# Kernel optimization log

Hardware: AMD Instinct MI355X
Metric: run time of the kernel (lower is better)

## Reference

```python
import jax, jax.numpy as jnp
import numpy as np

N, T, D, H = 100000, 16, 8, 40
HP1 = H + 1
ALPHA_DP = 1.0
KAPPA0 = 1000.0   # priorGaussianVarKappa
NU0 = 100.0       # priorWishartNu
PSI0_SCALE = 500.0  # priorWishartPsi = 500*I


def setup_inputs() -> dict:
    key = jax.random.key(0)
    ks = jax.random.split(key, 6)
    return {
        "BetaGamma1": jnp.ones((1, T), jnp.float32),
        "Phi": jax.random.uniform(ks[0], (N, T), jnp.float32),
        "inputData": jax.random.normal(ks[1], (N, D), jnp.float32),
        "outputData": jax.random.normal(ks[2], (N, 1), jnp.float32),
        "weightELM": jax.random.uniform(ks[3], (D, H), jnp.float32) * 2.0 - 1.0,
        "biasELM": jax.random.normal(ks[4], (H, 1), jnp.float32),
        "epsilonA": jnp.ones((1, T), jnp.float32),
        "epsilonB": jnp.ones((1, T), jnp.float32),
        "zetaA": 1e-4 * jnp.ones((1, T), jnp.float32),
        "zetaB": jnp.ones((1, T), jnp.float32),
    }


def reference(BetaGamma1, Phi, inputData, outputData, weightELM, biasELM,
              epsilonA, epsilonB, zetaA, zetaB):
    f32 = jnp.float32
    mu0 = jnp.zeros((D, 1), f32)                      # priorGaussianMeanMu
    Psi0 = PSI0_SCALE * jnp.eye(D, dtype=f32)         # priorWishartPsi

    sumPhi = jnp.sum(Phi, axis=0, keepdims=True)      # [1,T]

    # stick-breaking Beta params. Torch builds a flipped [T,N,T] tril mask;
    # mathematically BetaGamma2[t] = alpha + sum_{j>t} sum_n Phi[n,j]
    BetaGamma1_new = jnp.ones_like(BetaGamma1) + sumPhi
    col = sumPhi[0]                                   # [T]
    rev_incl = jnp.cumsum(col[::-1])[::-1]            # sum_{j>=t}
    BetaGamma2 = (ALPHA_DP + (rev_incl - col))[None, :]

    # Gaussian-Wishart natural-parameter updates.
    # Torch loops over clusters doing [N,D,D] bmm outer products; this is
    # S[:,:,t] = sum_n Phi[n,t] x_n x_n^T
    S = jnp.einsum('nt,ni,nj->ijt', Phi, inputData, inputData)  # [D,D,T]
    t11 = -0.5 * (Psi0 + KAPPA0 * mu0 @ mu0.T)[:, :, None] - 0.5 * S
    t12 = KAPPA0 * mu0 + inputData.T @ Phi            # [D,T]
    t21 = -0.5 * sumPhi - 0.5 * (NU0 + D + 2)         # [1,T]
    kappa = KAPPA0 + sumPhi                           # [1,T]
    mu = t12 / kappa                                  # [D,T]
    nu = -2.0 * t21 - 2.0 - float(D)                  # [1,T]
    psi = -2.0 * t11 - kappa[0][None, None, :] * jnp.einsum('it,jt->ijt', mu, mu)

    # ELM feature map + augmented design matrix X = [sigmoid(x W + b), 1]
    hmap = jax.nn.sigmoid(inputData @ weightELM + biasELM.T)   # [N,H]
    X = jnp.concatenate([hmap, jnp.ones((inputData.shape[0], 1), f32)], axis=1)  # [N,HP1]

    epsExp = (epsilonA / epsilonB)[0]                 # [T]
    zetaExp = (zetaA / zetaB)[0]                      # [T]

    # A[t] = X^T diag(Phi[:,t]) X   (torch: per-cluster bmm with diag_embed)
    A = jnp.einsum('nt,ni,nj->tij', Phi, X, X)        # [T,HP1,HP1]
    WS = jnp.linalg.inv(epsExp[:, None, None] * A
                        + zetaExp[:, None, None] * jnp.eye(HP1, dtype=f32))
    # b[t] = X^T diag(Phi[:,t]) y
    b = jnp.einsum('ni,nt->ti', X * outputData, Phi)  # [T,HP1]
    WMv = zetaExp[:, None] * jnp.einsum('tij,tj->ti', WS, b)   # [T,HP1]
    WM = WMv[:, :, None]                              # [T,HP1,1]

    # prior Zeta/Epsilon alias the variational initial values in __init__
    zetaA_new = zetaA + (H + 1) * 0.5
    zetaB_new = zetaB + 0.5 * (jnp.sum(WMv * WMv, axis=1)
                               + jnp.trace(WS, axis1=-2, axis2=-1))[None, :]
    epsA_new = epsilonA + 0.5 * sumPhi

    pred = jnp.einsum('ni,ti->tn', X, WMv)            # [T,N]
    err = outputData.T - pred                          # [T,N]
    t1 = jnp.einsum('tn,nt->t', err * err, Phi)[None, :]
    t2 = jnp.einsum('tij,tji->t', A, WS)[None, :]
    epsB_new = epsilonB + 0.5 * (t1 + t2)

    return (BetaGamma1_new, BetaGamma2, mu, kappa, nu, psi,
            WM, WS, zetaA_new, zetaB_new, epsA_new, epsB_new)
```

## Files before the change

kernel.cpp:

```cpp
#include <hip/hip_runtime.h>

#define Nn 100000
#define Tt 16
#define Dd 8
#define Hh 40
#define HP1 41

#define CSZ 53248
#define XEH_OFF  0
#define XEL_OFF  (XEH_OFF + 32 * Nn)
#define PHIT_OFF (XEL_OFF + 32 * Nn)
#define PART_OFF (PHIT_OFF + 16 * Nn)
#define P_OFF    (PART_OFF + 8 * CSZ)

#define OFF_BG1   0
#define OFF_BG2   16
#define OFF_MU    32
#define OFF_KAPPA 160
#define OFF_NU    176
#define OFF_PSI   192
#define OFF_WM    1216
#define OFF_WS    1872
#define OFF_ZA    28768
#define OFF_ZB    28784
#define OFF_EA    28800
#define OFF_EB    28816

typedef _Float16 f16x8 __attribute__((ext_vector_type(8)));
typedef float f32x4 __attribute__((ext_vector_type(4)));
typedef unsigned int u32x4 __attribute__((ext_vector_type(4)));

#define AIDX(i, t, j) ((((i) * 16 + (t)) * 64) + (j))

__global__ __launch_bounds__(256)
void elm_expand(const float* __restrict__ Phi, const float* __restrict__ Xd,
                const float* __restrict__ Yd, const float* __restrict__ W,
                const float* __restrict__ bb,
                unsigned short* __restrict__ XeHi, unsigned short* __restrict__ XeLo,
                float* __restrict__ PhiT)
{
  __shared__ float sW[Dd * Hh];
  __shared__ float sb[Hh];
  __shared__ float xs[64][9];
  __shared__ float ys[64];
  __shared__ float hrow[64][41];
  __shared__ float pt[16][68];
  int tid = threadIdx.x;
  int n0 = blockIdx.x * 64;

  for (int i = tid; i < Dd * Hh; i += 256) sW[i] = W[i];
  if (tid < Hh) sb[tid] = bb[tid];
  if (tid < 128) {
    int nl = tid >> 1, h4 = (tid & 1) * 4;
    int gn = n0 + nl;
    float4 v = (gn < Nn) ? *(const float4*)(Xd + (size_t)gn * 8 + h4)
                         : make_float4(0.f, 0.f, 0.f, 0.f);
    xs[nl][h4 + 0] = v.x; xs[nl][h4 + 1] = v.y;
    xs[nl][h4 + 2] = v.z; xs[nl][h4 + 3] = v.w;
  }
  if (tid < 64) { int gn = n0 + tid; ys[tid] = (gn < Nn) ? Yd[gn] : 0.f; }
  {
    int nl = tid >> 2, q = tid & 3;
    int gn = n0 + nl;
    float4 v = (gn < Nn) ? *(const float4*)(Phi + (size_t)gn * 16 + q * 4)
                         : make_float4(0.f, 0.f, 0.f, 0.f);
    pt[q * 4 + 0][nl] = v.x; pt[q * 4 + 1][nl] = v.y;
    pt[q * 4 + 2][nl] = v.z; pt[q * 4 + 3][nl] = v.w;
  }
  __syncthreads();
  {
    int nl = tid >> 2, hq = (tid & 3) * 10;
    for (int hh = 0; hh < 10; ++hh) {
      int h = hq + hh;
      float z = sb[h];
#pragma unroll
      for (int d = 0; d < 8; ++d) z = fmaf(xs[nl][d], sW[d * Hh + h], z);
      hrow[nl][h] = 1.f / (1.f + __expf(-z));
    }
  }
  __syncthreads();
  {
    int t = tid & 15, nq = tid >> 4;
    int gn = n0 + nq * 4;
    if (gn < Nn) {
      float4 v = make_float4(pt[t][nq * 4 + 0], pt[t][nq * 4 + 1],
                             pt[t][nq * 4 + 2], pt[t][nq * 4 + 3]);
      *(float4*)(PhiT + (size_t)t * Nn + gn) = v;
    }
  }
  {
    int cidx = tid >> 2, seg = tid & 3;
    int nl0 = seg * 16;
    float vv[16];
#pragma unroll
    for (int j = 0; j < 16; ++j) {
      int n = nl0 + j;
      float v;
      if (cidx < Hh) v = hrow[n][cidx];
      else if (cidx == 40) v = 1.f;
      else if (cidx < 49) v = xs[n][cidx - 41];
      else if (cidx == 49) v = ys[n];
      else v = 0.f;
      vv[j] = v;
    }
    unsigned short hs[16], ls[16];
#pragma unroll
    for (int j = 0; j < 16; ++j) {
      _Float16 h = (_Float16)vv[j];
      float r = vv[j] - (float)h;
      _Float16 lo = (_Float16)r;
      hs[j] = __builtin_bit_cast(unsigned short, h);
      ls[j] = __builtin_bit_cast(unsigned short, lo);
    }
#pragma unroll
    for (int q2 = 0; q2 < 2; ++q2) {
      int gn = n0 + nl0 + q2 * 8;
      if (gn < Nn) {
        uint4 uh, ul;
        uh.x = hs[q2*8+0] | ((unsigned)hs[q2*8+1] << 16);
        uh.y = hs[q2*8+2] | ((unsigned)hs[q2*8+3] << 16);
        uh.z = hs[q2*8+4] | ((unsigned)hs[q2*8+5] << 16);
        uh.w = hs[q2*8+6] | ((unsigned)hs[q2*8+7] << 16);
        ul.x = ls[q2*8+0] | ((unsigned)ls[q2*8+1] << 16);
        ul.y = ls[q2*8+2] | ((unsigned)ls[q2*8+3] << 16);
        ul.z = ls[q2*8+4] | ((unsigned)ls[q2*8+5] << 16);
        ul.w = ls[q2*8+6] | ((unsigned)ls[q2*8+7] << 16);
        *(uint4*)(XeHi + (size_t)cidx * Nn + gn) = uh;
        *(uint4*)(XeLo + (size_t)cidx * Nn + gn) = ul;
      }
    }
  }
}

__device__ __forceinline__ void gload16(const void* g, void* l) {
  __builtin_amdgcn_global_load_lds(
      (const __attribute__((address_space(1))) unsigned int*)g,
      (__attribute__((address_space(3))) unsigned int*)l, 16, 0, 0);
}

__global__ __launch_bounds__(512, 2)
void gram_mfma(const float* __restrict__ PhiT,
               const unsigned short* __restrict__ XeHi,
               const unsigned short* __restrict__ XeLo,
               float* __restrict__ P, int CH)
{
  __shared__ __align__(16) char smem[2][10240];

  int tid = threadIdx.x;
  int c = blockIdx.x;
  int l = tid & 63, w = tid >> 6;
  int l15 = l & 15, lg = l >> 4;
  int n0 = c * CH;
  int rem = Nn - n0; if (rem > CH) rem = CH;
  int nsteps = rem >> 5;

  int MT  = (w < 4) ? 7 : 6;
  int i0w = (w < 4) ? 7 * w : 28 + 6 * (w - 4);

  const char* g0; const char* g1 = nullptr;
  int ld0 = tid * 16, ld1 = (512 + tid) * 16;
  {
    int r = (tid & 255) >> 2, s = tid & 3;
    const unsigned short* bp = (tid < 256) ? XeHi : XeLo;
    g0 = (const char*)(bp + (size_t)r * Nn + n0 + 8 * (s ^ (r & 3)));
    if (tid < 128) {
      int t = tid >> 3, s2 = tid & 7;
      g1 = (const char*)(PhiT + (size_t)t * Nn + n0 + 4 * (s2 ^ (t & 7)));
    }
  }

#define STAGE(buf) do {                              \
    char* db = &smem[buf][0];                        \
    gload16(g0, db + ld0); g0 += 64;                 \
    if (tid < 128) { gload16(g1, db + ld1); g1 += 128; } \
  } while (0)

  int off_b[4];
#pragma unroll
  for (int nt = 0; nt < 4; ++nt) {
    int j = l15 + 16 * nt;
    off_b[nt] = j * 64 + 16 * (lg ^ (j & 3));
  }
  int off_p0 = 8192 + l15 * 128 + 16 * ((2 * lg) ^ (l15 & 7));
  int off_p1 = 8192 + l15 * 128 + 16 * ((2 * lg + 1) ^ (l15 & 7));
  int off_a[7];
#pragma unroll
  for (int mi = 0; mi < 7; ++mi) {
    int i = i0w + mi;
    off_a[mi] = i * 64 + 16 * (lg ^ (i & 3));
  }

  f32x4 acc[7][4];
#pragma unroll
  for (int mi = 0; mi < 7; ++mi)
#pragma unroll
    for (int nt = 0; nt < 4; ++nt) acc[mi][nt] = (f32x4){0.f, 0.f, 0.f, 0.f};

  STAGE(0);
  __syncthreads();

  for (int s = 0; s < nsteps; ++s) {
    int cur = s & 1;
    if (s + 1 < nsteps) STAGE(cur ^ 1);

    const char* base = &smem[cur][0];
    f32x4 p0 = *(const f32x4*)(base + off_p0);
    f32x4 p1 = *(const f32x4*)(base + off_p1);
    float ph[8] = {p0[0], p0[1], p0[2], p0[3], p1[0], p1[1], p1[2], p1[3]};

    f16x8 bh[4], bl[4];
#pragma unroll
    for (int nt = 0; nt < 4; ++nt) {
      bh[nt] = *(const f16x8*)(base + off_b[nt]);
      bl[nt] = *(const f16x8*)(base + 4096 + off_b[nt]);
    }
#pragma unroll
    for (int mi = 0; mi < 7; ++mi) {
      if (mi >= MT) break;
      f16x8 xh = *(const f16x8*)(base + off_a[mi]);
      f16x8 xl = *(const f16x8*)(base + 4096 + off_a[mi]);
      float v0 = ph[0] * ((float)xh[0] + (float)xl[0]);
      float v1 = ph[1] * ((float)xh[1] + (float)xl[1]);
      float v2 = ph[2] * ((float)xh[2] + (float)xl[2]);
      float v3 = ph[3] * ((float)xh[3] + (float)xl[3]);
      float v4 = ph[4] * ((float)xh[4] + (float)xl[4]);
      float v5 = ph[5] * ((float)xh[5] + (float)xl[5]);
      float v6 = ph[6] * ((float)xh[6] + (float)xl[6]);
      float v7 = ph[7] * ((float)xh[7] + (float)xl[7]);
      auto h0 = __builtin_amdgcn_cvt_pkrtz(v0, v1);
      auto h1 = __builtin_amdgcn_cvt_pkrtz(v2, v3);
      auto h2 = __builtin_amdgcn_cvt_pkrtz(v4, v5);
      auto h3 = __builtin_amdgcn_cvt_pkrtz(v6, v7);
      float r0 = v0 - (float)h0[0], r1 = v1 - (float)h0[1];
      float r2 = v2 - (float)h1[0], r3 = v3 - (float)h1[1];
      float r4 = v4 - (float)h2[0], r5 = v5 - (float)h2[1];
      float r6 = v6 - (float)h3[0], r7 = v7 - (float)h3[1];
      auto e0 = __builtin_amdgcn_cvt_pkrtz(r0, r1);
      auto e1 = __builtin_amdgcn_cvt_pkrtz(r2, r3);
      auto e2 = __builtin_amdgcn_cvt_pkrtz(r4, r5);
      auto e3 = __builtin_amdgcn_cvt_pkrtz(r6, r7);
      u32x4 uh = {__builtin_bit_cast(unsigned int, h0), __builtin_bit_cast(unsigned int, h1),
                  __builtin_bit_cast(unsigned int, h2), __builtin_bit_cast(unsigned int, h3)};
      u32x4 ul = {__builtin_bit_cast(unsigned int, e0), __builtin_bit_cast(unsigned int, e1),
                  __builtin_bit_cast(unsigned int, e2), __builtin_bit_cast(unsigned int, e3)};
      f16x8 ah = __builtin_bit_cast(f16x8, uh);
      f16x8 al = __builtin_bit_cast(f16x8, ul);
#pragma unroll
      for (int nt = 0; nt < 4; ++nt) {
        acc[mi][nt] = __builtin_amdgcn_mfma_f32_16x16x32_f16(ah, bh[nt], acc[mi][nt], 0, 0, 0);
        acc[mi][nt] = __builtin_amdgcn_mfma_f32_16x16x32_f16(ah, bl[nt], acc[mi][nt], 0, 0, 0);
        acc[mi][nt] = __builtin_amdgcn_mfma_f32_16x16x32_f16(al, bh[nt], acc[mi][nt], 0, 0, 0);
      }
    }
    __syncthreads();
  }
#undef STAGE

  float* Pc = P + (size_t)c * CSZ;
#pragma unroll
  for (int mi = 0; mi < 7; ++mi) {
    if (mi >= MT) break;
    int i = i0w + mi;
#pragma unroll
    for (int nt = 0; nt < 4; ++nt) {
      int j = nt * 16 + l15;
#pragma unroll
      for (int r = 0; r < 4; ++r)
        Pc[(i * 16 + lg * 4 + r) * 64 + j] = acc[mi][nt][r];
    }
  }
}

__global__ __launch_bounds__(256)
void reduce_a(const float4* __restrict__ P4, int nchunks, float4* __restrict__ part4)
{
  int g = blockIdx.y;
  int idx = blockIdx.x * 256 + threadIdx.x;
  int per = (nchunks + 7) / 8;
  int c0 = g * per, c1 = c0 + per; if (c1 > nchunks) c1 = nchunks;
  float4 s = make_float4(0.f, 0.f, 0.f, 0.f);
  for (int cc = c0; cc < c1; ++cc) {
    float4 v = P4[(size_t)cc * (CSZ / 4) + idx];
    s.x += v.x; s.y += v.y; s.z += v.z; s.w += v.w;
  }
  part4[(size_t)g * (CSZ / 4) + idx] = s;
}

__device__ __forceinline__ float accv(const float* __restrict__ part, int idx) {
  float s = 0.f;
#pragma unroll
  for (int g = 0; g < 8; ++g) s += part[g * CSZ + idx];
  return s;
}

__global__ __launch_bounds__(256)
void finalize_kernel(const float* __restrict__ part, const float* __restrict__ epsA,
                     const float* __restrict__ epsB, const float* __restrict__ zetA,
                     const float* __restrict__ zetB, float* __restrict__ out)
{
  int t = blockIdx.x;
  int tid = threadIdx.x;
  __shared__ float G[HP1][84];
  __shared__ float As[HP1][HP1 + 1];
  __shared__ float bs[HP1];
  __shared__ float colk[HP1];
  __shared__ float red[256];
  __shared__ float wmv[HP1];
  __shared__ float rowv[4][HP1 + 1];
  __shared__ float mus[Dd];

  float epsExp = epsA[t] / epsB[t];
  float zetaExp = zetA[t] / zetB[t];

  for (int idx = tid; idx < HP1 * HP1; idx += 256) {
    int i = idx / HP1, j = idx % HP1;
    float a = accv(part, AIDX(i, t, j));
    As[i][j] = a;
    G[i][j] = epsExp * a + (i == j ? zetaExp : 0.f);
    G[i][41 + j] = (i == j) ? 1.f : 0.f;
  }
  for (int idx = tid; idx < HP1; idx += 256) {
    G[idx][82] = 0.f; G[idx][83] = 0.f;
    bs[idx] = accv(part, AIDX(idx, t, 49));
  }
  __syncthreads();

  int c = tid % HP1;
  int ig = tid / HP1;
  int irow0 = ig * 7;

  for (int k = 0; k < HP1; ++k) {
    float pivinv = 1.f / G[k][k];
    if (tid >= 1 && tid <= HP1) G[k][k + tid] *= pivinv;
    if (tid < HP1) colk[tid] = (tid == k) ? 0.f : G[tid][k];
    __syncthreads();
    if (ig < 6) {
      int j = k + 1 + c;
      float pk = G[k][j];
#pragma unroll
      for (int r = 0; r < 7; ++r) {
        int i = irow0 + r;
        if (i < HP1 && i != k) G[i][j] = fmaf(-colk[i], pk, G[i][j]);
      }
    }
    __syncthreads();
  }

  for (int idx = tid; idx < HP1 * HP1; idx += 256) {
    int i = idx / HP1, j = idx % HP1;
    out[OFF_WS + (t * HP1 + i) * HP1 + j] = G[i][41 + j];
  }
  if (tid < HP1) {
    float s = 0.f;
    for (int j = 0; j < HP1; ++j) s += G[tid][41 + j] * bs[j];
    float w = zetaExp * s;
    wmv[tid] = w;
    out[OFF_WM + t * HP1 + tid] = w;
  }
  __syncthreads();
  float lt2 = 0.f;
  for (int idx = tid; idx < HP1 * HP1; idx += 256) {
    int i = idx / HP1, j = idx % HP1;
    lt2 += As[i][j] * G[i][41 + j];
  }
  red[tid] = lt2; __syncthreads();
  for (int s = 128; s > 0; s >>= 1) {
    if (tid < s) red[tid] += red[tid + s];
    __syncthreads();
  }
  float t2v = red[0];
  if (tid < HP1) {
    float w = wmv[tid];
    float aw = 0.f;
    for (int j = 0; j < HP1; ++j) aw += As[tid][j] * wmv[j];
    rowv[0][tid] = w * bs[tid];
    rowv[1][tid] = w * w;
    rowv[2][tid] = G[tid][41 + tid];
    rowv[3][tid] = w * aw;
  }
  __syncthreads();

  float sp = accv(part, AIDX(40, t, 40));
  float kap = 1000.f + sp;
  float syy = accv(part, AIDX(49, t, 49));

  if (tid == 0) {
    float wb = 0.f, wn = 0.f, trc = 0.f, quad = 0.f;
    for (int i = 0; i < HP1; ++i) {
      wb += rowv[0][i]; wn += rowv[1][i]; trc += rowv[2][i]; quad += rowv[3][i];
    }
    float t1 = syy - 2.f * wb + quad;
    out[OFF_BG1 + t] = 1.f + sp;
    float rest = 0.f;
    for (int u = t + 1; u < Tt; ++u) rest += accv(part, AIDX(40, u, 40));
    out[OFF_BG2 + t] = 1.f + rest;
    out[OFF_KAPPA + t] = kap;
    out[OFF_NU + t] = sp + 100.f;
    out[OFF_ZA + t] = zetA[t] + 0.5f * (float)HP1;
    out[OFF_ZB + t] = zetB[t] + 0.5f * (wn + trc);
    out[OFF_EA + t] = epsA[t] + 0.5f * sp;
    out[OFF_EB + t] = epsB[t] + 0.5f * (t1 + t2v);
  }
  if (tid < Dd) {
    float m = accv(part, AIDX(40, t, 41 + tid)) / kap;
    mus[tid] = m;
    out[OFF_MU + tid * Tt + t] = m;
  }
  __syncthreads();
  if (tid < Dd * Dd) {
    int i = tid / Dd, j = tid % Dd;
    float S = accv(part, AIDX(41 + i, t, 41 + j));
    float v = (i == j ? 500.f : 0.f) + S - kap * mus[i] * mus[j];
    out[OFF_PSI + (i * Dd + j) * Tt + t] = v;
  }
}

extern "C" void kernel_launch(void* const* d_in, const int* in_sizes, int n_in,
                              void* d_out, int out_size, void* d_ws, size_t ws_size,
                              hipStream_t stream) {
  const float* Phi = (const float*)d_in[1];
  const float* Xd  = (const float*)d_in[2];
  const float* Yd  = (const float*)d_in[3];
  const float* W   = (const float*)d_in[4];
  const float* bb  = (const float*)d_in[5];
  const float* eA  = (const float*)d_in[6];
  const float* eB  = (const float*)d_in[7];
  const float* zA  = (const float*)d_in[8];
  const float* zB  = (const float*)d_in[9];
  float* out = (float*)d_out;
  float* ws  = (float*)d_ws;

  unsigned short* XeHi = (unsigned short*)(ws + XEH_OFF);
  unsigned short* XeLo = (unsigned short*)(ws + XEL_OFF);
  float* PhiT = ws + PHIT_OFF;
  float* part = ws + PART_OFF;
  float* P    = ws + P_OFF;

  long maxChunks = ((long)(ws_size / 4) - (long)P_OFF) / CSZ;
  if (maxChunks < 1) maxChunks = 1;
  long cap = maxChunks < 256 ? maxChunks : 256;
  long sp = (3125 + cap - 1) / cap;
  int CH = (int)(32 * sp);
  int KCe = (Nn + CH - 1) / CH;

  hipLaunchKernelGGL(elm_expand, dim3((Nn + 63) / 64), dim3(256), 0, stream,
                     Phi, Xd, Yd, W, bb, XeHi, XeLo, PhiT);
  hipLaunchKernelGGL(gram_mfma, dim3(KCe), dim3(512), 0, stream,
                     PhiT, XeHi, XeLo, P, CH);
  hipLaunchKernelGGL(reduce_a, dim3(52, 8), dim3(256), 0, stream,
                     (const float4*)P, KCe, (float4*)part);
  hipLaunchKernelGGL(finalize_kernel, dim3(Tt), dim3(256), 0, stream,
                     part, eA, eB, zA, zB, out);
}
```

Before: 170.6 us.

## Deepen gram MFMA pipeline to 4 stages with chunk-wide Phi preload

Restructures the gram MFMA kernel to use a 4-buffer LDS ring with three stages of loads in flight, managed by explicit vmcnt waits and raw barriers instead of double buffering with __syncthreads. Each chunk's Phi tile is loaded into LDS once up front. Chunk size is fixed at compile time, and a grid-stride loop lets the grid be capped by workspace size. MFMA sections run at raised wave priority via s_setprio. The aim is to hide global-load latency and cut barrier stalls. The cost is more LDS per block, which may limit occupancy.

Result: no change. 170.5 us (-0.1%).

```diff
diff --git a/kernel.cpp b/kernel.cpp
--- a/kernel.cpp
+++ b/kernel.cpp
@@ -5,6 +5,10 @@
 #define Dd 8
 #define Hh 40
 #define HP1 41
+
+#define SPC 13
+#define CH  (32 * SPC)
+#define KCMAX ((Nn + CH - 1) / CH)
 
 #define CSZ 53248
 #define XEH_OFF  0
@@ -138,42 +142,23 @@
       (__attribute__((address_space(3))) unsigned int*)l, 16, 0, 0);
 }
 
+#define PHI_LDS 32768
+#define LDS_BYTES (PHI_LDS + 16 * CH * 4)
+
 __global__ __launch_bounds__(512, 2)
 void gram_mfma(const float* __restrict__ PhiT,
                const unsigned short* __restrict__ XeHi,
                const unsigned short* __restrict__ XeLo,
-               float* __restrict__ P, int CH)
+               float* __restrict__ P)
 {
-  __shared__ __align__(16) char smem[2][10240];
+  __shared__ __align__(16) char smem[LDS_BYTES];
 
   int tid = threadIdx.x;
-  int c = blockIdx.x;
   int l = tid & 63, w = tid >> 6;
   int l15 = l & 15, lg = l >> 4;
-  int n0 = c * CH;
-  int rem = Nn - n0; if (rem > CH) rem = CH;
-  int nsteps = rem >> 5;
 
   int MT  = (w < 4) ? 7 : 6;
   int i0w = (w < 4) ? 7 * w : 28 + 6 * (w - 4);
-
-  const char* g0; const char* g1 = nullptr;
-  int ld0 = tid * 16, ld1 = (512 + tid) * 16;
-  {
-    int r = (tid & 255) >> 2, s = tid & 3;
-    const unsigned short* bp = (tid < 256) ? XeHi : XeLo;
-    g0 = (const char*)(bp + (size_t)r * Nn + n0 + 8 * (s ^ (r & 3)));
-    if (tid < 128) {
-      int t = tid >> 3, s2 = tid & 7;
-      g1 = (const char*)(PhiT + (size_t)t * Nn + n0 + 4 * (s2 ^ (t & 7)));
-    }
-  }
-
-#define STAGE(buf) do {                              \
-    char* db = &smem[buf][0];                        \
-    gload16(g0, db + ld0); g0 += 64;                 \
-    if (tid < 128) { gload16(g1, db + ld1); g1 += 128; } \
-  } while (0)
 
   int off_b[4];
 #pragma unroll
@@ -181,14 +166,17 @@
     int j = l15 + 16 * nt;
     off_b[nt] = j * 64 + 16 * (lg ^ (j & 3));
   }
-  int off_p0 = 8192 + l15 * 128 + 16 * ((2 * lg) ^ (l15 & 7));
-  int off_p1 = 8192 + l15 * 128 + 16 * ((2 * lg + 1) ^ (l15 & 7));
   int off_a[7];
 #pragma unroll
   for (int mi = 0; mi < 7; ++mi) {
     int i = i0w + mi;
     off_a[mi] = i * 64 + 16 * (lg ^ (i & 3));
   }
+  int off_p0 = l15 * 128 + 16 * ((2 * lg) ^ (l15 & 7));
+  int off_p1 = l15 * 128 + 16 * ((2 * lg + 1) ^ (l15 & 7));
+  int ld0 = tid * 16;
+  int brow = (tid & 255) >> 2, bsl = tid & 3;
+  const unsigned short* bplane = (tid < 256) ? XeHi : XeLo;
 
   f32x4 acc[7][4];
 #pragma unroll
@@ -196,67 +184,98 @@
 #pragma unroll
     for (int nt = 0; nt < 4; ++nt) acc[mi][nt] = (f32x4){0.f, 0.f, 0.f, 0.f};
 
-  STAGE(0);
-  __syncthreads();
-
-  for (int s = 0; s < nsteps; ++s) {
-    int cur = s & 1;
-    if (s + 1 < nsteps) STAGE(cur ^ 1);
-
-    const char* base = &smem[cur][0];
-    f32x4 p0 = *(const f32x4*)(base + off_p0);
-    f32x4 p1 = *(const f32x4*)(base + off_p1);
-    float ph[8] = {p0[0], p0[1], p0[2], p0[3], p1[0], p1[1], p1[2], p1[3]};
-
-    f16x8 bh[4], bl[4];
-#pragma unroll
-    for (int nt = 0; nt < 4; ++nt) {
-      bh[nt] = *(const f16x8*)(base + off_b[nt]);
-      bl[nt] = *(const f16x8*)(base + 4096 + off_b[nt]);
-    }
-#pragma unroll
-    for (int mi = 0; mi < 7; ++mi) {
-      if (mi >= MT) break;
-      f16x8 xh = *(const f16x8*)(base + off_a[mi]);
-      f16x8 xl = *(const f16x8*)(base + 4096 + off_a[mi]);
-      float v0 = ph[0] * ((float)xh[0] + (float)xl[0]);
-      float v1 = ph[1] * ((float)xh[1] + (float)xl[1]);
-      float v2 = ph[2] * ((float)xh[2] + (float)xl[2]);
-      float v3 = ph[3] * ((float)xh[3] + (float)xl[3]);
-      float v4 = ph[4] * ((float)xh[4] + (float)xl[4]);
-      float v5 = ph[5] * ((float)xh[5] + (float)xl[5]);
-      float v6 = ph[6] * ((float)xh[6] + (float)xl[6]);
-      float v7 = ph[7] * ((float)xh[7] + (float)xl[7]);
-      auto h0 = __builtin_amdgcn_cvt_pkrtz(v0, v1);
-      auto h1 = __builtin_amdgcn_cvt_pkrtz(v2, v3);
-      auto h2 = __builtin_amdgcn_cvt_pkrtz(v4, v5);
-      auto h3 = __builtin_amdgcn_cvt_pkrtz(v6, v7);
-      float r0 = v0 - (float)h0[0], r1 = v1 - (float)h0[1];
-      float r2 = v2 - (float)h1[0], r3 = v3 - (float)h1[1];
-      float r4 = v4 - (float)h2[0], r5 = v5 - (float)h2[1];
-      float r6 = v6 - (float)h3[0], r7 = v7 - (float)h3[1];
-      auto e0 = __builtin_amdgcn_cvt_pkrtz(r0, r1);
-      auto e1 = __builtin_amdgcn_cvt_pkrtz(r2, r3);
-      auto e2 = __builtin_amdgcn_cvt_pkrtz(r4, r5);
-      auto e3 = __builtin_amdgcn_cvt_pkrtz(r6, r7);
-      u32x4 uh = {__builtin_bit_cast(unsigned int, h0), __builtin_bit_cast(unsigned int, h1),
-                  __builtin_bit_cast(unsigned int, h2), __builtin_bit_cast(unsigned int, h3)};
-      u32x4 ul = {__builtin_bit_cast(unsigned int, e0), __builtin_bit_cast(unsigned int, e1),
-                  __builtin_bit_cast(unsigned int, e2), __builtin_bit_cast(unsigned int, e3)};
-      f16x8 ah = __builtin_bit_cast(f16x8, uh);
-      f16x8 al = __builtin_bit_cast(f16x8, ul);
+  for (int cc = blockIdx.x; cc < KCMAX; cc += gridDim.x) {
+    int n0 = cc * CH;
+    int rem = Nn - n0; if (rem > CH) rem = CH;
+    int nsteps = rem >> 5;
+
+    __builtin_amdgcn_s_barrier();
+    asm volatile("" ::: "memory");
+
+    const char* gB = (const char*)(bplane + (size_t)brow * Nn + n0
+                                   + 8 * (bsl ^ (brow & 3)));
+#define STAGE(sx) gload16(gB + (size_t)(sx) * 64, \
+                          &smem[(((sx) & 3) * 8192) + ld0])
+
+#pragma unroll
+    for (int q = 0; q < 4; ++q) {
+      int gp = tid + q * 512;
+      if (gp < 16 * CH / 4) {
+        int s = gp >> 7, qq = gp & 127, t = qq >> 3, sl = qq & 7;
+        gload16(PhiT + (size_t)t * Nn + n0 + s * 32 + 4 * (sl ^ (t & 7)),
+                &smem[PHI_LDS + gp * 16]);
+      }
+    }
+    STAGE(0);
+    if (nsteps > 1) STAGE(1);
+    if (nsteps > 2) STAGE(2);
+
+    for (int s = 0; s < nsteps; ++s) {
+      int out = nsteps - 1 - s; if (out > 2) out = 2;
+      if (out == 2)      asm volatile("s_waitcnt vmcnt(2)" ::: "memory");
+      else if (out == 1) asm volatile("s_waitcnt vmcnt(1)" ::: "memory");
+      else               asm volatile("s_waitcnt vmcnt(0)" ::: "memory");
+      __builtin_amdgcn_s_barrier();
+      asm volatile("" ::: "memory");
+      if (s + 3 < nsteps) STAGE(s + 3);
+
+      const char* base  = &smem[(s & 3) * 8192];
+      const char* pbase = &smem[PHI_LDS + s * 2048];
+      f32x4 p0 = *(const f32x4*)(pbase + off_p0);
+      f32x4 p1 = *(const f32x4*)(pbase + off_p1);
+      float ph[8] = {p0[0], p0[1], p0[2], p0[3], p1[0], p1[1], p1[2], p1[3]};
+
+      f16x8 bh[4], bl[4];
 #pragma unroll
       for (int nt = 0; nt < 4; ++nt) {
-        acc[mi][nt] = __builtin_amdgcn_mfma_f32_16x16x32_f16(ah, bh[nt], acc[mi][nt], 0, 0, 0);
-        acc[mi][nt] = __builtin_amdgcn_mfma_f32_16x16x32_f16(ah, bl[nt], acc[mi][nt], 0, 0, 0);
-        acc[mi][nt] = __builtin_amdgcn_mfma_f32_16x16x32_f16(al, bh[nt], acc[mi][nt], 0, 0, 0);
+        bh[nt] = *(const f16x8*)(base + off_b[nt]);
+        bl[nt] = *(const f16x8*)(base + 4096 + off_b[nt]);
       }
-    }
-    __syncthreads();
-  }
+      __builtin_amdgcn_s_setprio(1);
+#pragma unroll
+      for (int mi = 0; mi < 7; ++mi) {
+        if (mi >= MT) break;
+        f16x8 xh = *(const f16x8*)(base + off_a[mi]);
+        f16x8 xl = *(const f16x8*)(base + 4096 + off_a[mi]);
+        float v0 = ph[0] * ((float)xh[0] + (float)xl[0]);
+        float v1 = ph[1] * ((float)xh[1] + (float)xl[1]);
+        float v2 = ph[2] * ((float)xh[2] + (float)xl[2]);
+        float v3 = ph[3] * ((float)xh[3] + (float)xl[3]);
+        float v4 = ph[4] * ((float)xh[4] + (float)xl[4]);
+        float v5 = ph[5] * ((float)xh[5] + (float)xl[5]);
+        float v6 = ph[6] * ((float)xh[6] + (float)xl[6]);
+        float v7 = ph[7] * ((float)xh[7] + (float)xl[7]);
+        auto h0 = __builtin_amdgcn_cvt_pkrtz(v0, v1);
+        auto h1 = __builtin_amdgcn_cvt_pkrtz(v2, v3);
+        auto h2 = __builtin_amdgcn_cvt_pkrtz(v4, v5);
+        auto h3 = __builtin_amdgcn_cvt_pkrtz(v6, v7);
+        float r0 = v0 - (float)h0[0], r1 = v1 - (float)h0[1];
+        float r2 = v2 - (float)h1[0], r3 = v3 - (float)h1[1];
+        float r4 = v4 - (float)h2[0], r5 = v5 - (float)h2[1];
+        float r6 = v6 - (float)h3[0], r7 = v7 - (float)h3[1];
+        auto e0 = __builtin_amdgcn_cvt_pkrtz(r0, r1);
+        auto e1 = __builtin_amdgcn_cvt_pkrtz(r2, r3);
+        auto e2 = __builtin_amdgcn_cvt_pkrtz(r4, r5);
+        auto e3 = __builtin_amdgcn_cvt_pkrtz(r6, r7);
+        u32x4 uh = {__builtin_bit_cast(unsigned int, h0), __builtin_bit_cast(unsigned int, h1),
+                    __builtin_bit_cast(unsigned int, h2), __builtin_bit_cast(unsigned int, h3)};
+        u32x4 ul = {__builtin_bit_cast(unsigned int, e0), __builtin_bit_cast(unsigned int, e1),
+                    __builtin_bit_cast(unsigned int, e2), __builtin_bit_cast(unsigned int, e3)};
+        f16x8 ah = __builtin_bit_cast(f16x8, uh);
+        f16x8 al = __builtin_bit_cast(f16x8, ul);
+#pragma unroll
+        for (int nt = 0; nt < 4; ++nt) {
+          acc[mi][nt] = __builtin_amdgcn_mfma_f32_16x16x32_f16(ah, bh[nt], acc[mi][nt], 0, 0, 0);
+          acc[mi][nt] = __builtin_amdgcn_mfma_f32_16x16x32_f16(ah, bl[nt], acc[mi][nt], 0, 0, 0);
+          acc[mi][nt] = __builtin_amdgcn_mfma_f32_16x16x32_f16(al, bh[nt], acc[mi][nt], 0, 0, 0);
+        }
+      }
+      __builtin_amdgcn_s_setprio(0);
+    }
 #undef STAGE
-
-  float* Pc = P + (size_t)c * CSZ;
+  }
+
+  float* Pc = P + (size_t)blockIdx.x * CSZ;
 #pragma unroll
   for (int mi = 0; mi < 7; ++mi) {
     if (mi >= MT) break;
@@ -272,12 +291,12 @@
 }
 
 __global__ __launch_bounds__(256)
-void reduce_a(const float4* __restrict__ P4, int nchunks, float4* __restrict__ part4)
+void reduce_a(const float4* __restrict__ P4, int nslabs, float4* __restrict__ part4)
 {
   int g = blockIdx.y;
   int idx = blockIdx.x * 256 + threadIdx.x;
-  int per = (nchunks + 7) / 8;
-  int c0 = g * per, c1 = c0 + per; if (c1 > nchunks) c1 = nchunks;
+  int per = (nslabs + 7) / 8;
+  int c0 = g * per, c1 = c0 + per; if (c1 > nslabs) c1 = nslabs;
   float4 s = make_float4(0.f, 0.f, 0.f, 0.f);
   for (int cc = c0; cc < c1; ++cc) {
     float4 v = P4[(size_t)cc * (CSZ / 4) + idx];
@@ -436,19 +455,16 @@
   float* part = ws + PART_OFF;
   float* P    = ws + P_OFF;
 
-  long maxChunks = ((long)(ws_size / 4) - (long)P_OFF) / CSZ;
-  if (maxChunks < 1) maxChunks = 1;
-  long cap = maxChunks < 256 ? maxChunks : 256;
-  long sp = (3125 + cap - 1) / cap;
-  int CH = (int)(32 * sp);
-  int KCe = (Nn + CH - 1) / CH;
+  long maxSlabs = ((long)(ws_size / 4) - (long)P_OFF) / CSZ;
+  int grid1 = (int)(maxSlabs < KCMAX ? maxSlabs : KCMAX);
+  if (grid1 < 1) grid1 = 1;
 
   hipLaunchKernelGGL(elm_expand, dim3((Nn + 63) / 64), dim3(256), 0, stream,
                      Phi, Xd, Yd, W, bb, XeHi, XeLo, PhiT);
-  hipLaunchKernelGGL(gram_mfma, dim3(KCe), dim3(512), 0, stream,
-                     PhiT, XeHi, XeLo, P, CH);
+  hipLaunchKernelGGL(gram_mfma, dim3(grid1), dim3(512), 0, stream,
+                     PhiT, XeHi, XeLo, P);
   hipLaunchKernelGGL(reduce_a, dim3(52, 8), dim3(256), 0, stream,
-                     (const float4*)P, KCe, (float4*)part);
+                     (const float4*)P, grid1, (float4*)part);
   hipLaunchKernelGGL(finalize_kernel, dim3(Tt), dim3(256), 0, stream,
                      part, eA, eB, zA, zB, out);
 }
```

## Store packed upper-triangular Gram partials and retune LDS swizzle and chunk count

Applied to the files above, without the earlier changes.

Each gram chunk now writes only the upper triangle of the symmetric 50x50 per-cluster Gram matrix in a packed layout (1275 pairs x 16 clusters) instead of the full 64x16x64 tile. This cuts partial-sum write and reduce traffic, so the chunk cap rises from 256 to 391 blocks and reduce_a gets a smaller grid. It also changes the LDS XOR swizzle to use (row>>1)&3 and raises wave priority around the MFMA loop. Finalize looks up entries through a symmetric packed index, which adds some index arithmetic.

After: 186.1 us. 9.1% more time.

```diff
diff --git a/kernel.cpp b/kernel.cpp
--- a/kernel.cpp
+++ b/kernel.cpp
@@ -6,12 +6,14 @@
 #define Hh 40
 #define HP1 41
 
-#define CSZ 53248
+#define NPAIR 1275
+#define PSZ (NPAIR * 16)
+
 #define XEH_OFF  0
 #define XEL_OFF  (XEH_OFF + 32 * Nn)
 #define PHIT_OFF (XEL_OFF + 32 * Nn)
 #define PART_OFF (PHIT_OFF + 16 * Nn)
-#define P_OFF    (PART_OFF + 8 * CSZ)
+#define P_OFF    (PART_OFF + 8 * PSZ)
 
 #define OFF_BG1   0
 #define OFF_BG2   16
@@ -30,7 +32,10 @@
 typedef float f32x4 __attribute__((ext_vector_type(4)));
 typedef unsigned int u32x4 __attribute__((ext_vector_type(4)));
 
-#define AIDX(i, t, j) ((((i) * 16 + (t)) * 64) + (j))
+__device__ __forceinline__ int pidx(int i, int j) {
+  if (i > j) { int tmp = i; i = j; j = tmp; }
+  return (i * (2 * 50 - i + 1)) / 2 + (j - i);
+}
 
 __global__ __launch_bounds__(256)
 void elm_expand(const float* __restrict__ Phi, const float* __restrict__ Xd,
@@ -162,7 +167,7 @@
   {
     int r = (tid & 255) >> 2, s = tid & 3;
     const unsigned short* bp = (tid < 256) ? XeHi : XeLo;
-    g0 = (const char*)(bp + (size_t)r * Nn + n0 + 8 * (s ^ (r & 3)));
+    g0 = (const char*)(bp + (size_t)r * Nn + n0 + 8 * (s ^ ((r >> 1) & 3)));
     if (tid < 128) {
       int t = tid >> 3, s2 = tid & 7;
       g1 = (const char*)(PhiT + (size_t)t * Nn + n0 + 4 * (s2 ^ (t & 7)));
@@ -179,7 +184,7 @@
 #pragma unroll
   for (int nt = 0; nt < 4; ++nt) {
     int j = l15 + 16 * nt;
-    off_b[nt] = j * 64 + 16 * (lg ^ (j & 3));
+    off_b[nt] = j * 64 + 16 * (lg ^ ((j >> 1) & 3));
   }
   int off_p0 = 8192 + l15 * 128 + 16 * ((2 * lg) ^ (l15 & 7));
   int off_p1 = 8192 + l15 * 128 + 16 * ((2 * lg + 1) ^ (l15 & 7));
@@ -187,7 +192,7 @@
 #pragma unroll
   for (int mi = 0; mi < 7; ++mi) {
     int i = i0w + mi;
-    off_a[mi] = i * 64 + 16 * (lg ^ (i & 3));
+    off_a[mi] = i * 64 + 16 * (lg ^ ((i >> 1) & 3));
   }
 
   f32x4 acc[7][4];
@@ -214,6 +219,7 @@
       bh[nt] = *(const f16x8*)(base + off_b[nt]);
       bl[nt] = *(const f16x8*)(base + 4096 + off_b[nt]);
     }
+    __builtin_amdgcn_s_setprio(1);
 #pragma unroll
     for (int mi = 0; mi < 7; ++mi) {
       if (mi >= MT) break;
@@ -252,44 +258,49 @@
         acc[mi][nt] = __builtin_amdgcn_mfma_f32_16x16x32_f16(al, bh[nt], acc[mi][nt], 0, 0, 0);
       }
     }
+    __builtin_amdgcn_s_setprio(0);
     __syncthreads();
   }
 #undef STAGE
 
-  float* Pc = P + (size_t)c * CSZ;
+  float* Pc = P + (size_t)c * PSZ;
 #pragma unroll
   for (int mi = 0; mi < 7; ++mi) {
     if (mi >= MT) break;
     int i = i0w + mi;
-#pragma unroll
-    for (int nt = 0; nt < 4; ++nt) {
-      int j = nt * 16 + l15;
-#pragma unroll
-      for (int r = 0; r < 4; ++r)
-        Pc[(i * 16 + lg * 4 + r) * 64 + j] = acc[mi][nt][r];
+    if (i < 50) {
+#pragma unroll
+      for (int nt = 0; nt < 4; ++nt) {
+        int j = nt * 16 + l15;
+        if (j >= i && j < 50) {
+          int pb = (i * (101 - i)) / 2 + (j - i);
+          *(f32x4*)(Pc + pb * 16 + lg * 4) = acc[mi][nt];
+        }
+      }
     }
   }
 }
 
 __global__ __launch_bounds__(256)
-void reduce_a(const float4* __restrict__ P4, int nchunks, float4* __restrict__ part4)
+void reduce_a(const float4* __restrict__ P4, int nslabs, float4* __restrict__ part4)
 {
   int g = blockIdx.y;
   int idx = blockIdx.x * 256 + threadIdx.x;
-  int per = (nchunks + 7) / 8;
-  int c0 = g * per, c1 = c0 + per; if (c1 > nchunks) c1 = nchunks;
+  if (idx >= PSZ / 4) return;
+  int per = (nslabs + 7) / 8;
+  int c0 = g * per, c1 = c0 + per; if (c1 > nslabs) c1 = nslabs;
   float4 s = make_float4(0.f, 0.f, 0.f, 0.f);
   for (int cc = c0; cc < c1; ++cc) {
-    float4 v = P4[(size_t)cc * (CSZ / 4) + idx];
+    float4 v = P4[(size_t)cc * (PSZ / 4) + idx];
     s.x += v.x; s.y += v.y; s.z += v.z; s.w += v.w;
   }
-  part4[(size_t)g * (CSZ / 4) + idx] = s;
+  part4[(size_t)g * (PSZ / 4) + idx] = s;
 }
 
 __device__ __forceinline__ float accv(const float* __restrict__ part, int idx) {
   float s = 0.f;
 #pragma unroll
-  for (int g = 0; g < 8; ++g) s += part[g * CSZ + idx];
+  for (int g = 0; g < 8; ++g) s += part[g * PSZ + idx];
   return s;
 }
 
@@ -314,14 +325,14 @@
 
   for (int idx = tid; idx < HP1 * HP1; idx += 256) {
     int i = idx / HP1, j = idx % HP1;
-    float a = accv(part, AIDX(i, t, j));
+    float a = accv(part, pidx(i, j) * Tt + t);
     As[i][j] = a;
     G[i][j] = epsExp * a + (i == j ? zetaExp : 0.f);
     G[i][41 + j] = (i == j) ? 1.f : 0.f;
   }
   for (int idx = tid; idx < HP1; idx += 256) {
     G[idx][82] = 0.f; G[idx][83] = 0.f;
-    bs[idx] = accv(part, AIDX(idx, t, 49));
+    bs[idx] = accv(part, pidx(idx, 49) * Tt + t);
   }
   __syncthreads();
 
@@ -380,9 +391,9 @@
   }
   __syncthreads();
 
-  float sp = accv(part, AIDX(40, t, 40));
+  float sp = accv(part, pidx(40, 40) * Tt + t);
   float kap = 1000.f + sp;
-  float syy = accv(part, AIDX(49, t, 49));
+  float syy = accv(part, pidx(49, 49) * Tt + t);
 
   if (tid == 0) {
     float wb = 0.f, wn = 0.f, trc = 0.f, quad = 0.f;
@@ -392,7 +403,7 @@
     float t1 = syy - 2.f * wb + quad;
     out[OFF_BG1 + t] = 1.f + sp;
     float rest = 0.f;
-    for (int u = t + 1; u < Tt; ++u) rest += accv(part, AIDX(40, u, 40));
+    for (int u = t + 1; u < Tt; ++u) rest += accv(part, pidx(40, 40) * Tt + u);
     out[OFF_BG2 + t] = 1.f + rest;
     out[OFF_KAPPA + t] = kap;
     out[OFF_NU + t] = sp + 100.f;
@@ -402,14 +413,14 @@
     out[OFF_EB + t] = epsB[t] + 0.5f * (t1 + t2v);
   }
   if (tid < Dd) {
-    float m = accv(part, AIDX(40, t, 41 + tid)) / kap;
+    float m = accv(part, pidx(40, 41 + tid) * Tt + t) / kap;
     mus[tid] = m;
     out[OFF_MU + tid * Tt + t] = m;
   }
   __syncthreads();
   if (tid < Dd * Dd) {
     int i = tid / Dd, j = tid % Dd;
-    float S = accv(part, AIDX(41 + i, t, 41 + j));
+    float S = accv(part, pidx(41 + i, 41 + j) * Tt + t);
     float v = (i == j ? 500.f : 0.f) + S - kap * mus[i] * mus[j];
     out[OFF_PSI + (i * Dd + j) * Tt + t] = v;
   }
@@ -436,9 +447,9 @@
   float* part = ws + PART_OFF;
   float* P    = ws + P_OFF;
 
-  long maxChunks = ((long)(ws_size / 4) - (long)P_OFF) / CSZ;
+  long maxChunks = ((long)(ws_size / 4) - (long)P_OFF) / PSZ;
   if (maxChunks < 1) maxChunks = 1;
-  long cap = maxChunks < 256 ? maxChunks : 256;
+  long cap = maxChunks < 391 ? maxChunks : 391;
   long sp = (3125 + cap - 1) / cap;
   int CH = (int)(32 * sp);
   int KCe = (Nn + CH - 1) / CH;
@@ -447,7 +458,7 @@
                      Phi, Xd, Yd, W, bb, XeHi, XeLo, PhiT);
   hipLaunchKernelGGL(gram_mfma, dim3(KCe), dim3(512), 0, stream,
                      PhiT, XeHi, XeLo, P, CH);
-  hipLaunchKernelGGL(reduce_a, dim3(52, 8), dim3(256), 0, stream,
+  hipLaunchKernelGGL(reduce_a, dim3(20, 8), dim3(256), 0, stream,
                      (const float4*)P, KCe, (float4*)part);
   hipLaunchKernelGGL(finalize_kernel, dim3(Tt), dim3(256), 0, stream,
                      part, eA, eB, zA, zB, out);
```
